# Kernel tuning notes

Hardware: AMD Instinct MI355X
Metric: run time of the kernel (lower is better)

Reference implementation:

```python
import jax, jax.numpy as jnp
import numpy as np

EPS = 1e-5  # torch BatchNorm1d default eps

def _bn(x, g, b, m, v):
    # eval-mode BatchNorm1d with running statistics
    return (x - m) * jax.lax.rsqrt(v + EPS) * g + b

def setup_inputs() -> dict:
    key = jax.random.key(0)
    ks = jax.random.split(key, 6)
    N, E, D = 10000, 320000, 128
    h = jax.random.normal(ks[0], (N, D), dtype=jnp.float32)
    src = jax.random.randint(ks[1], (E,), 0, N)
    dst = jax.random.randint(ks[2], (E,), 0, N)
    # Linear weights (torch layout: [out, in]), kaiming-ish scale
    W0 = jax.random.normal(ks[3], (128, 256), dtype=jnp.float32) * (1.0 / np.sqrt(256))
    b0 = jnp.zeros((128,), jnp.float32)
    W1 = jax.random.normal(ks[4], (128, 128), dtype=jnp.float32) * (1.0 / np.sqrt(128))
    b1 = jnp.zeros((128,), jnp.float32)
    W2 = jax.random.normal(ks[5], (1, 128), dtype=jnp.float32) * (1.0 / np.sqrt(128))
    b2 = jnp.zeros((1,), jnp.float32)
    # BatchNorm affine params + running stats per layer input size
    g0, be0, m0, v0 = jnp.ones((256,)), jnp.zeros((256,)), jnp.zeros((256,)), jnp.ones((256,))
    g1, be1, m1, v1 = jnp.ones((128,)), jnp.zeros((128,)), jnp.zeros((128,)), jnp.ones((128,))
    g2, be2, m2, v2 = jnp.ones((128,)), jnp.zeros((128,)), jnp.zeros((128,)), jnp.ones((128,))
    return dict(h=h, src=src, dst=dst, W0=W0, b0=b0, W1=W1, b1=b1, W2=W2, b2=b2,
                g0=g0, be0=be0, g1=g1, be1=be1, g2=g2, be2=be2,
                m0=m0, v0=v0, m1=m1, v1=v1, m2=m2, v2=v2)

def reference(h, src, dst, W0, b0, W1, b1, W2, b2,
              g0, be0, g1, be1, g2, be2, m0, v0, m1, v1, m2, v2):
    # edge gather + concat: [E, 2*D]
    x = jnp.concatenate([h[src], h[dst]], axis=1)
    # stage 0: BN -> Linear (dropout is identity in eval)
    x = _bn(x, g0, be0, m0, v0) @ W0.T + b0
    # stage 1: ReLU -> BN -> Linear
    x = jax.nn.relu(x)
    x = _bn(x, g1, be1, m1, v1) @ W1.T + b1
    # stage 2: ReLU -> BN -> Linear
    x = jax.nn.relu(x)
    x = _bn(x, g2, be2, m2, v2) @ W2.T + b2
    return x  # [E, 1] edge scores
```

## Files before the change

### kernel.cpp

```cpp
#include <hip/hip_runtime.h>
#include <hip/hip_bf16.h>

#define BN_EPS 1e-5f

typedef short bf16x8 __attribute__((ext_vector_type(8)));
typedef float f32x4  __attribute__((ext_vector_type(4)));

static __device__ __forceinline__ unsigned short f2bf(float f) {
    union { float f; unsigned int u; } v; v.f = f;
    unsigned int u = v.u;
    unsigned int r = (u + 0x7FFFu + ((u >> 16) & 1u)) >> 16;
    return (unsigned short)r;
}

static __device__ __forceinline__ unsigned short f2bf_hw(float f) {
    __hip_bfloat16 b = __float2bfloat16(f);
    union { __hip_bfloat16 b; unsigned short u; } v; v.b = b;
    return v.u;
}

__global__ __launch_bounds__(256) void k_prep(
        const float* __restrict__ h, unsigned short* __restrict__ hb, int n4, int nCvt,
        const float* __restrict__ W0, const float* __restrict__ b0,
        const float* __restrict__ W1, const float* __restrict__ b1,
        const float* __restrict__ W2, const float* __restrict__ b2,
        const float* __restrict__ g0, const float* __restrict__ be0,
        const float* __restrict__ m0, const float* __restrict__ v0,
        const float* __restrict__ g1, const float* __restrict__ be1,
        const float* __restrict__ m1, const float* __restrict__ v1,
        const float* __restrict__ g2, const float* __restrict__ be2,
        const float* __restrict__ m2, const float* __restrict__ v2,
        unsigned short* __restrict__ W0sw, unsigned short* __restrict__ W1sw,
        float* __restrict__ b0f, float* __restrict__ b1f,
        float* __restrict__ w2f, float* __restrict__ b2f) {
    const int b = blockIdx.x;
    const int tid = threadIdx.x;

    if (b < nCvt) {
        int i = b * 256 + tid;
        if (i < n4) {
            float4 f = ((const float4*)h)[i];
            ushort4 o;
            o.x = f2bf(f.x); o.y = f2bf(f.y); o.z = f2bf(f.z); o.w = f2bf(f.w);
            ((ushort4*)hb)[i] = o;
        }
        return;
    }
    int br = b - nCvt;
    if (br < 128) {
        int t = br * 256 + tid;
        int j = t & 7, lane = (t >> 3) & 63, nt = (t >> 9) & 7, kb = t >> 12;
        int k = kb * 32 + (lane >> 4) * 8 + j;
        int n = nt * 16 + (lane & 15);
        float s = g0[k] * rsqrtf(v0[k] + BN_EPS);
        W0sw[t] = f2bf(W0[n * 256 + k] * s);
        return;
    }
    br -= 128;
    if (br < 64) {
        int t = br * 256 + tid;
        int j = t & 7, lane = (t >> 3) & 63, nt = (t >> 9) & 7, kb = t >> 12;
        int k = kb * 32 + (lane >> 4) * 8 + j;
        int n = nt * 16 + (lane & 15);
        float s = g1[k] * rsqrtf(v1[k] + BN_EPS);
        W1sw[t] = f2bf(W1[n * 128 + k] * s);
        return;
    }
    br -= 64;
    {
        if (tid >= 64) return;
        const int i = br, lane = tid;
        float s0 = 0.f;
#pragma unroll
        for (int c = 0; c < 4; c++) {
            int k = c * 64 + lane;
            float sc = g0[k] * rsqrtf(v0[k] + BN_EPS);
            s0 += W0[i * 256 + k] * (be0[k] - m0[k] * sc);
        }
        float s1 = 0.f;
#pragma unroll
        for (int c = 0; c < 2; c++) {
            int k = c * 64 + lane;
            float sc = g1[k] * rsqrtf(v1[k] + BN_EPS);
            s1 += W1[i * 128 + k] * (be1[k] - m1[k] * sc);
        }
        float s2 = 0.f;
        if (i == 0) {
#pragma unroll
            for (int c = 0; c < 2; c++) {
                int k = c * 64 + lane;
                float sc = g2[k] * rsqrtf(v2[k] + BN_EPS);
                s2 += W2[k] * (be2[k] - m2[k] * sc);
            }
        }
#pragma unroll
        for (int off = 1; off < 64; off <<= 1) {
            s0 += __shfl_xor(s0, off);
            s1 += __shfl_xor(s1, off);
            s2 += __shfl_xor(s2, off);
        }
        if (lane == 0) {
            b0f[i] = b0[i] + s0;
            b1f[i] = b1[i] + s1;
            w2f[i] = W2[i] * (g2[i] * rsqrtf(v2[i] + BN_EPS));
            if (i == 0) b2f[0] = b2[0] + s2;
        }
    }
}

__global__ __launch_bounds__(256, 3) void k_main(
        const int* __restrict__ src, const int* __restrict__ dst,
        const unsigned short* __restrict__ hb,
        const unsigned short* __restrict__ W0sw, const unsigned short* __restrict__ W1sw,
        const float* __restrict__ b0f, const float* __restrict__ b1f,
        const float* __restrict__ w2f, const float* __restrict__ b2fp,
        float* __restrict__ out, int E, int nGroups) {
    __shared__ __align__(16) unsigned short Abuf[4 * 2 * 4 * 64 * 8];
    __shared__ __align__(16) unsigned short x1S[4][4][64][8];
    __shared__ float pS[4][64];

    const int tid  = threadIdx.x;
    const int wave = tid >> 6;
    const int lane = tid & 63;
    const int quad = lane >> 4;
    const int m    = lane & 15;

    bf16x8 B0[8][2], B1[4][2];
#pragma unroll
    for (int kb = 0; kb < 8; kb++)
#pragma unroll
        for (int hh = 0; hh < 2; hh++)
            B0[kb][hh] = *(const bf16x8*)(W0sw + ((kb * 8 + (wave * 2 + hh)) * 64 + lane) * 8);
#pragma unroll
    for (int kb = 0; kb < 4; kb++)
#pragma unroll
        for (int hh = 0; hh < 2; hh++)
            B1[kb][hh] = *(const bf16x8*)(W1sw + ((kb * 8 + (wave * 2 + hh)) * 64 + lane) * 8);

    float b0v[2], b1v[2], w2v[2];
#pragma unroll
    for (int hh = 0; hh < 2; hh++) {
        int n = (wave * 2 + hh) * 16 + m;
        b0v[hh] = b0f[n];
        b1v[hh] = b1f[n];
        w2v[hh] = w2f[n];
    }
    const float b2s = *b2fp;
    const int stride = gridDim.x;

    int gi = blockIdx.x;
    int rSn, rDn;
    {
        int e = gi * 64 + wave * 16 + m;
        if (e >= E) e = E - 1;
        rSn = src[e];
        rDn = dst[e];
#pragma unroll
        for (int half = 0; half < 2; half++) {
            int row = half ? rDn : rSn;
#pragma unroll
            for (int kb4 = 0; kb4 < 4; kb4++) {
                const unsigned short* gp = hb + (size_t)row * 128 + kb4 * 32 + quad * 8;
                unsigned short* lp = Abuf + ((wave * 2 + half) * 4 + kb4) * 512 + lane * 8;
                __builtin_amdgcn_global_load_lds(
                    (const __attribute__((address_space(1))) void*)gp,
                    (__attribute__((address_space(3))) void*)lp, 16, 0, 0);
            }
        }
    }

    int prevE = -1;
    for (; gi < nGroups; gi += stride) {
        __syncthreads();

        if (prevE >= 0 && wave == 0) {
            int e = prevE + lane;
            if (e < E)
                out[e] = pS[0][lane] + pS[1][lane] + pS[2][lane] + pS[3][lane] + b2s;
        }

        int nextGi = gi + stride;
        {
            int en = (nextGi < nGroups ? nextGi : gi) * 64 + wave * 16 + m;
            if (en >= E) en = E - 1;
            rSn = src[en];
            rDn = dst[en];
        }

        f32x4 acc0[4][2];
#pragma unroll
        for (int g = 0; g < 4; g++)
#pragma unroll
            for (int hh = 0; hh < 2; hh++) acc0[g][hh] = (f32x4){0.f, 0.f, 0.f, 0.f};

#pragma unroll
        for (int kb = 0; kb < 8; kb++) {
            bf16x8 a[4];
#pragma unroll
            for (int g = 0; g < 4; g++)
                a[g] = *(const bf16x8*)(Abuf + ((g * 2 + (kb >> 2)) * 4 + (kb & 3)) * 512 + lane * 8);
#pragma unroll
            for (int hh = 0; hh < 2; hh++)
#pragma unroll
                for (int g = 0; g < 4; g++)
                    acc0[g][hh] = __builtin_amdgcn_mfma_f32_16x16x32_bf16(a[g], B0[kb][hh], acc0[g][hh], 0, 0, 0);
        }

#pragma unroll
        for (int g = 0; g < 4; g++) {
#pragma unroll
            for (int hh = 0; hh < 2; hh++) {
                int qp = (hh << 1) | (m >> 3);
                int j  = m & 7;
#pragma unroll
                for (int r = 0; r < 4; r++) {
                    float v = acc0[g][hh][r] + b0v[hh];
                    v = v > 0.f ? v : 0.f;
                    x1S[g][wave][qp * 16 + quad * 4 + r][j] = f2bf_hw(v);
                }
            }
        }
        __syncthreads();

        if (nextGi < nGroups) {
#pragma unroll
            for (int half = 0; half < 2; half++) {
                int row = half ? rDn : rSn;
#pragma unroll
                for (int kb4 = 0; kb4 < 4; kb4++) {
                    const unsigned short* gp = hb + (size_t)row * 128 + kb4 * 32 + quad * 8;
                    unsigned short* lp = Abuf + ((wave * 2 + half) * 4 + kb4) * 512 + lane * 8;
                    __builtin_amdgcn_global_load_lds(
                        (const __attribute__((address_space(1))) void*)gp,
                        (__attribute__((address_space(3))) void*)lp, 16, 0, 0);
                }
            }
        }

        f32x4 acc1[4][2];
#pragma unroll
        for (int g = 0; g < 4; g++)
#pragma unroll
            for (int hh = 0; hh < 2; hh++) acc1[g][hh] = (f32x4){0.f, 0.f, 0.f, 0.f};

#pragma unroll
        for (int kb = 0; kb < 4; kb++) {
            bf16x8 a[4];
#pragma unroll
            for (int g = 0; g < 4; g++)
                a[g] = *(const bf16x8*)&x1S[g][kb][lane][0];
#pragma unroll
            for (int hh = 0; hh < 2; hh++)
#pragma unroll
                for (int g = 0; g < 4; g++)
                    acc1[g][hh] = __builtin_amdgcn_mfma_f32_16x16x32_bf16(a[g], B1[kb][hh], acc1[g][hh], 0, 0, 0);
        }

#pragma unroll
        for (int g = 0; g < 4; g++) {
            float s[4] = {0.f, 0.f, 0.f, 0.f};
#pragma unroll
            for (int hh = 0; hh < 2; hh++)
#pragma unroll
                for (int r = 0; r < 4; r++) {
                    float v = acc1[g][hh][r] + b1v[hh];
                    v = v > 0.f ? v : 0.f;
                    s[r] += v * w2v[hh];
                }
#pragma unroll
            for (int off = 1; off < 16; off <<= 1)
#pragma unroll
                for (int r = 0; r < 4; r++) s[r] += __shfl_xor(s[r], off, 16);
            if (m == 0) {
#pragma unroll
                for (int r = 0; r < 4; r++) pS[wave][g * 16 + quad * 4 + r] = s[r];
            }
        }
        prevE = gi * 64;
    }

    __syncthreads();
    if (prevE >= 0 && wave == 0) {
        int e = prevE + lane;
        if (e < E)
            out[e] = pS[0][lane] + pS[1][lane] + pS[2][lane] + pS[3][lane] + b2s;
    }
}

extern "C" void kernel_launch(void* const* d_in, const int* in_sizes, int n_in,
                              void* d_out, int out_size, void* d_ws, size_t ws_size,
                              hipStream_t stream) {
    const float* h   = (const float*)d_in[0];
    const int*   src = (const int*)d_in[1];
    const int*   dst = (const int*)d_in[2];
    const float* W0  = (const float*)d_in[3];
    const float* b0  = (const float*)d_in[4];
    const float* W1  = (const float*)d_in[5];
    const float* b1  = (const float*)d_in[6];
    const float* W2  = (const float*)d_in[7];
    const float* b2  = (const float*)d_in[8];
    const float* g0  = (const float*)d_in[9];
    const float* be0 = (const float*)d_in[10];
    const float* g1  = (const float*)d_in[11];
    const float* be1 = (const float*)d_in[12];
    const float* g2  = (const float*)d_in[13];
    const float* be2 = (const float*)d_in[14];
    const float* m0  = (const float*)d_in[15];
    const float* v0  = (const float*)d_in[16];
    const float* m1  = (const float*)d_in[17];
    const float* v1  = (const float*)d_in[18];
    const float* m2  = (const float*)d_in[19];
    const float* v2  = (const float*)d_in[20];
    float* out = (float*)d_out;

    const int hsz = in_sizes[0];
    const int E   = in_sizes[1];

    char* ws = (char*)d_ws;
    size_t off = (size_t)hsz * 2;
    off = (off + 255) & ~(size_t)255;
    unsigned short* hb   = (unsigned short*)ws;
    unsigned short* W0sw = (unsigned short*)(ws + off);  off += 65536;
    unsigned short* W1sw = (unsigned short*)(ws + off);  off += 32768;
    float* b0f = (float*)(ws + off);  off += 512;
    float* b1f = (float*)(ws + off);  off += 512;
    float* w2f = (float*)(ws + off);  off += 512;
    float* b2f = (float*)(ws + off);  off += 16;

    int n4   = hsz / 4;
    int nCvt = (n4 + 255) / 256;
    int prepBlocks = nCvt + 128 + 64 + 128;
    k_prep<<<prepBlocks, 256, 0, stream>>>(h, hb, n4, nCvt,
                                           W0, b0, W1, b1, W2, b2,
                                           g0, be0, m0, v0, g1, be1, m1, v1,
                                           g2, be2, m2, v2,
                                           W0sw, W1sw, b0f, b1f, w2f, b2f);

    int nGroups = (E + 63) / 64;
    int nBlocks = nGroups < 768 ? nGroups : 768;
    k_main<<<nBlocks, 256, 0, stream>>>(src, dst, hb, W0sw, W1sw,
                                        b0f, b1f, w2f, b2f, out, E, nGroups);
}
```

Before: 143.6 us.

## Process 96 edges per block iteration to amortize register-resident weights

Each block iteration now handles 96 edges (six 16-row groups) instead of 64. Each wave runs MFMAs over all six groups against its register-held W0/W1 slices, and the gather loads are spread so waves 0-1 fetch two groups and waves 2-3 fetch one. Occupancy drops from 3 to 2 blocks per SIMD and the grid from 768 to 512 blocks. The per-edge partial sums now reuse x1S as scratch, with an extra barrier and an immediate write-out in place of the deferred pS write. This should raise MFMA work per barrier and per weight load, at the cost of latency hiding, uneven gather load across waves, and one more sync per iteration.

```diff
diff --git a/kernel.cpp b/kernel.cpp
--- a/kernel.cpp
+++ b/kernel.cpp
@@ -108,16 +108,15 @@
     }
 }
 
-__global__ __launch_bounds__(256, 3) void k_main(
+__global__ __launch_bounds__(256, 2) void k_main(
         const int* __restrict__ src, const int* __restrict__ dst,
         const unsigned short* __restrict__ hb,
         const unsigned short* __restrict__ W0sw, const unsigned short* __restrict__ W1sw,
         const float* __restrict__ b0f, const float* __restrict__ b1f,
         const float* __restrict__ w2f, const float* __restrict__ b2fp,
         float* __restrict__ out, int E, int nGroups) {
-    __shared__ __align__(16) unsigned short Abuf[4 * 2 * 4 * 64 * 8];
-    __shared__ __align__(16) unsigned short x1S[4][4][64][8];
-    __shared__ float pS[4][64];
+    __shared__ __align__(16) unsigned short Abuf[6 * 2 * 4 * 64 * 8];
+    __shared__ __align__(16) unsigned short x1S[6][4][64][8];
 
     const int tid  = threadIdx.x;
     const int wave = tid >> 6;
@@ -148,66 +147,79 @@
     const float b2s = *b2fp;
     const int stride = gridDim.x;
 
+    const int nMyG = (wave < 2) ? 2 : 1;
+    int myG0 = wave, myG1 = 4 + wave;
+
     int gi = blockIdx.x;
-    int rSn, rDn;
+    int rS0, rD0, rS1, rD1;
     {
-        int e = gi * 64 + wave * 16 + m;
-        if (e >= E) e = E - 1;
-        rSn = src[e];
-        rDn = dst[e];
-#pragma unroll
-        for (int half = 0; half < 2; half++) {
-            int row = half ? rDn : rSn;
-#pragma unroll
-            for (int kb4 = 0; kb4 < 4; kb4++) {
-                const unsigned short* gp = hb + (size_t)row * 128 + kb4 * 32 + quad * 8;
-                unsigned short* lp = Abuf + ((wave * 2 + half) * 4 + kb4) * 512 + lane * 8;
-                __builtin_amdgcn_global_load_lds(
-                    (const __attribute__((address_space(1))) void*)gp,
-                    (__attribute__((address_space(3))) void*)lp, 16, 0, 0);
-            }
-        }
-    }
-
-    int prevE = -1;
+        int e0 = gi * 96 + myG0 * 16 + m;
+        if (e0 >= E) e0 = E - 1;
+        rS0 = src[e0]; rD0 = dst[e0];
+        if (nMyG == 2) {
+            int e1 = gi * 96 + myG1 * 16 + m;
+            if (e1 >= E) e1 = E - 1;
+            rS1 = src[e1]; rD1 = dst[e1];
+        }
+#pragma unroll
+        for (int idx = 0; idx < 2; idx++) {
+            if (idx >= nMyG) break;
+            int g  = idx ? myG1 : myG0;
+            int rs = idx ? rS1 : rS0;
+            int rd = idx ? rD1 : rD0;
+#pragma unroll
+            for (int half = 0; half < 2; half++) {
+                int row = half ? rd : rs;
+#pragma unroll
+                for (int kb4 = 0; kb4 < 4; kb4++) {
+                    const unsigned short* gp = hb + (size_t)row * 128 + kb4 * 32 + quad * 8;
+                    unsigned short* lp = Abuf + ((g * 2 + half) * 4 + kb4) * 512 + lane * 8;
+                    __builtin_amdgcn_global_load_lds(
+                        (const __attribute__((address_space(1))) void*)gp,
+                        (__attribute__((address_space(3))) void*)lp, 16, 0, 0);
+                }
+            }
+        }
+    }
+
     for (; gi < nGroups; gi += stride) {
+        const int eBase = gi * 96;
         __syncthreads();
-
-        if (prevE >= 0 && wave == 0) {
-            int e = prevE + lane;
-            if (e < E)
-                out[e] = pS[0][lane] + pS[1][lane] + pS[2][lane] + pS[3][lane] + b2s;
-        }
 
         int nextGi = gi + stride;
         {
-            int en = (nextGi < nGroups ? nextGi : gi) * 64 + wave * 16 + m;
-            if (en >= E) en = E - 1;
-            rSn = src[en];
-            rDn = dst[en];
-        }
-
-        f32x4 acc0[4][2];
-#pragma unroll
-        for (int g = 0; g < 4; g++)
+            int eb = (nextGi < nGroups ? nextGi : gi) * 96;
+            int e0 = eb + myG0 * 16 + m;
+            if (e0 >= E) e0 = E - 1;
+            rS0 = src[e0]; rD0 = dst[e0];
+            if (nMyG == 2) {
+                int e1 = eb + myG1 * 16 + m;
+                if (e1 >= E) e1 = E - 1;
+                rS1 = src[e1]; rD1 = dst[e1];
+            }
+        }
+
+        f32x4 acc0[6][2];
+#pragma unroll
+        for (int g = 0; g < 6; g++)
 #pragma unroll
             for (int hh = 0; hh < 2; hh++) acc0[g][hh] = (f32x4){0.f, 0.f, 0.f, 0.f};
 
 #pragma unroll
         for (int kb = 0; kb < 8; kb++) {
-            bf16x8 a[4];
-#pragma unroll
-            for (int g = 0; g < 4; g++)
+            bf16x8 a[6];
+#pragma unroll
+            for (int g = 0; g < 6; g++)
                 a[g] = *(const bf16x8*)(Abuf + ((g * 2 + (kb >> 2)) * 4 + (kb & 3)) * 512 + lane * 8);
 #pragma unroll
             for (int hh = 0; hh < 2; hh++)
 #pragma unroll
-                for (int g = 0; g < 4; g++)
+                for (int g = 0; g < 6; g++)
                     acc0[g][hh] = __builtin_amdgcn_mfma_f32_16x16x32_bf16(a[g], B0[kb][hh], acc0[g][hh], 0, 0, 0);
         }
 
 #pragma unroll
-        for (int g = 0; g < 4; g++) {
+        for (int g = 0; g < 6; g++) {
 #pragma unroll
             for (int hh = 0; hh < 2; hh++) {
                 int qp = (hh << 1) | (m >> 3);
@@ -224,40 +236,47 @@
 
         if (nextGi < nGroups) {
 #pragma unroll
-            for (int half = 0; half < 2; half++) {
-                int row = half ? rDn : rSn;
-#pragma unroll
-                for (int kb4 = 0; kb4 < 4; kb4++) {
-                    const unsigned short* gp = hb + (size_t)row * 128 + kb4 * 32 + quad * 8;
-                    unsigned short* lp = Abuf + ((wave * 2 + half) * 4 + kb4) * 512 + lane * 8;
-                    __builtin_amdgcn_global_load_lds(
-                        (const __attribute__((address_space(1))) void*)gp,
-                        (__attribute__((address_space(3))) void*)lp, 16, 0, 0);
+            for (int idx = 0; idx < 2; idx++) {
+                if (idx >= nMyG) break;
+                int g  = idx ? myG1 : myG0;
+                int rs = idx ? rS1 : rS0;
+                int rd = idx ? rD1 : rD0;
+#pragma unroll
+                for (int half = 0; half < 2; half++) {
+                    int row = half ? rd : rs;
+#pragma unroll
+                    for (int kb4 = 0; kb4 < 4; kb4++) {
+                        const unsigned short* gp = hb + (size_t)row * 128 + kb4 * 32 + quad * 8;
+                        unsigned short* lp = Abuf + ((g * 2 + half) * 4 + kb4) * 512 + lane * 8;
+                        __builtin_amdgcn_global_load_lds(
+                            (const __attribute__((address_space(1))) void*)gp,
+                            (__attribute__((address_space(3))) void*)lp, 16, 0, 0);
+                    }
                 }
             }
         }
 
-        f32x4 acc1[4][2];
-#pragma unroll
-        for (int g = 0; g < 4; g++)
+        f32x4 acc1[6][2];
+#pragma unroll
+        for (int g = 0; g < 6; g++)
 #pragma unroll
             for (int hh = 0; hh < 2; hh++) acc1[g][hh] = (f32x4){0.f, 0.f, 0.f, 0.f};
 
 #pragma unroll
         for (int kb = 0; kb < 4; kb++) {
-            bf16x8 a[4];
-#pragma unroll
-            for (int g = 0; g < 4; g++)
+            bf16x8 a[6];
+#pragma unroll
+            for (int g = 0; g < 6; g++)
                 a[g] = *(const bf16x8*)&x1S[g][kb][lane][0];
 #pragma unroll
             for (int hh = 0; hh < 2; hh++)
 #pragma unroll
-                for (int g = 0; g < 4; g++)
+                for (int g = 0; g < 6; g++)
                     acc1[g][hh] = __builtin_amdgcn_mfma_f32_16x16x32_bf16(a[g], B1[kb][hh], acc1[g][hh], 0, 0, 0);
         }
 
 #pragma unroll
-        for (int g = 0; g < 4; g++) {
+        for (int g = 0; g < 6; g++) {
             float s[4] = {0.f, 0.f, 0.f, 0.f};
 #pragma unroll
             for (int hh = 0; hh < 2; hh++)
@@ -272,18 +291,23 @@
 #pragma unroll
                 for (int r = 0; r < 4; r++) s[r] += __shfl_xor(s[r], off, 16);
             if (m == 0) {
-#pragma unroll
-                for (int r = 0; r < 4; r++) pS[wave][g * 16 + quad * 4 + r] = s[r];
-            }
-        }
-        prevE = gi * 64;
-    }
-
-    __syncthreads();
-    if (prevE >= 0 && wave == 0) {
-        int e = prevE + lane;
-        if (e < E)
-            out[e] = pS[0][lane] + pS[1][lane] + pS[2][lane] + pS[3][lane] + b2s;
+                float* pS = (float*)&x1S[0][0][0][0];
+                pS[(wave * 6 + g) * 16 + quad * 4 + 0] = s[0];
+                pS[(wave * 6 + g) * 16 + quad * 4 + 1] = s[1];
+                pS[(wave * 6 + g) * 16 + quad * 4 + 2] = s[2];
+                pS[(wave * 6 + g) * 16 + quad * 4 + 3] = s[3];
+            }
+        }
+        __syncthreads();
+        {
+            int eo = wave * 64 + lane;
+            if (wave < 2 && eo < 96) {
+                const float* pS = (const float*)&x1S[0][0][0][0];
+                int e = eBase + eo;
+                if (e < E)
+                    out[e] = pS[0 * 96 + eo] + pS[1 * 96 + eo] + pS[2 * 96 + eo] + pS[3 * 96 + eo] + b2s;
+            }
+        }
     }
 }
 
@@ -336,8 +360,8 @@
                                            g2, be2, m2, v2,
                                            W0sw, W1sw, b0f, b1f, w2f, b2f);
 
-    int nGroups = (E + 63) / 64;
-    int nBlocks = nGroups < 768 ? nGroups : 768;
+    int nGroups = (E + 95) / 96;
+    int nBlocks = nGroups < 512 ? nGroups : 512;
     k_main<<<nBlocks, 256, 0, stream>>>(src, dst, hb, W0sw, W1sw,
                                         b0f, b1f, w2f, b2f, out, E, nGroups);
 }
```

New measurement: 149.1 us. 3.8% more time.

## Software-pipeline layer-0 and layer-1 across iterations with double-buffered LDS

Applied to the files above, without the earlier changes.

Restructures the main loop into a two-stage software pipeline. Each iteration runs layer-0 MFMAs for the current edge group and layer-1 for the previous group, using double-buffered A tiles, hidden activations and partial sums. That removes one __syncthreads per iteration, and the gather DMA for the next group is issued before compute rather than mid-iteration. Group size drops to 48 edges (3 MFMA row tiles) to fit the doubled LDS, with occupancy lowered to 2 blocks/SM and grid to 512. The trade-off is fewer edges per MFMA batch, lower occupancy, and prologue/epilogue complexity.

```diff
diff --git a/kernel.cpp b/kernel.cpp
--- a/kernel.cpp
+++ b/kernel.cpp
@@ -2,6 +2,8 @@
 #include <hip/hip_bf16.h>
 
 #define BN_EPS 1e-5f
+#define MG 3
+#define GEDGES 48
 
 typedef short bf16x8 __attribute__((ext_vector_type(8)));
 typedef float f32x4  __attribute__((ext_vector_type(4)));
@@ -108,16 +110,35 @@
     }
 }
 
-__global__ __launch_bounds__(256, 3) void k_main(
+static __device__ __forceinline__ void dma_issue(
+        unsigned short* AbufBase, const unsigned short* __restrict__ hb,
+        int wave, int lane, int quad, int rowS, int rowD) {
+    const int gIdx = (wave < 2) ? wave : 2;
+    const int h0 = (wave == 3) ? 1 : 0;
+    const int h1 = (wave < 2) ? 1 : h0;
+    for (int half = h0; half <= h1; half++) {
+        int row = half ? rowD : rowS;
+#pragma unroll
+        for (int kb4 = 0; kb4 < 4; kb4++) {
+            const unsigned short* gp = hb + (size_t)row * 128 + kb4 * 32 + quad * 8;
+            unsigned short* lp = AbufBase + ((gIdx * 2 + half) * 4 + kb4) * 512 + lane * 8;
+            __builtin_amdgcn_global_load_lds(
+                (const __attribute__((address_space(1))) void*)gp,
+                (__attribute__((address_space(3))) void*)lp, 16, 0, 0);
+        }
+    }
+}
+
+__global__ __launch_bounds__(256, 2) void k_main(
         const int* __restrict__ src, const int* __restrict__ dst,
         const unsigned short* __restrict__ hb,
         const unsigned short* __restrict__ W0sw, const unsigned short* __restrict__ W1sw,
         const float* __restrict__ b0f, const float* __restrict__ b1f,
         const float* __restrict__ w2f, const float* __restrict__ b2fp,
         float* __restrict__ out, int E, int nGroups) {
-    __shared__ __align__(16) unsigned short Abuf[4 * 2 * 4 * 64 * 8];
-    __shared__ __align__(16) unsigned short x1S[4][4][64][8];
-    __shared__ float pS[4][64];
+    __shared__ __align__(16) unsigned short Abuf[2][MG * 2 * 4 * 64 * 8];
+    __shared__ __align__(16) unsigned short x1S[2][MG][4][64][8];
+    __shared__ float pS[2][4][GEDGES];
 
     const int tid  = threadIdx.x;
     const int wave = tid >> 6;
@@ -147,67 +168,64 @@
     }
     const float b2s = *b2fp;
     const int stride = gridDim.x;
+    const int gIdx = (wave < 2) ? wave : 2;
 
     int gi = blockIdx.x;
-    int rSn, rDn;
+    int p = 0;
+    int eM1 = -1, eM2 = -1;
+    int rNS, rND;
+
     {
-        int e = gi * 64 + wave * 16 + m;
-        if (e >= E) e = E - 1;
-        rSn = src[e];
-        rDn = dst[e];
-#pragma unroll
-        for (int half = 0; half < 2; half++) {
-            int row = half ? rDn : rSn;
-#pragma unroll
-            for (int kb4 = 0; kb4 < 4; kb4++) {
-                const unsigned short* gp = hb + (size_t)row * 128 + kb4 * 32 + quad * 8;
-                unsigned short* lp = Abuf + ((wave * 2 + half) * 4 + kb4) * 512 + lane * 8;
-                __builtin_amdgcn_global_load_lds(
-                    (const __attribute__((address_space(1))) void*)gp,
-                    (__attribute__((address_space(3))) void*)lp, 16, 0, 0);
-            }
-        }
-    }
-
-    int prevE = -1;
-    for (; gi < nGroups; gi += stride) {
+        int eb = gi * GEDGES;
+        int e = eb + gIdx * 16 + m; if (e >= E) e = E - 1;
+        int rs = src[e], rd = dst[e];
+        dma_issue(&Abuf[0][0], hb, wave, lane, quad, rs, rd);
+        int gN = gi + stride;
+        int ebN = (gN < nGroups ? gN : gi) * GEDGES;
+        int eN = ebN + gIdx * 16 + m; if (eN >= E) eN = E - 1;
+        rNS = src[eN]; rND = dst[eN];
+    }
+
+    for (; gi < nGroups; gi += stride, p ^= 1) {
         __syncthreads();
 
-        if (prevE >= 0 && wave == 0) {
-            int e = prevE + lane;
+        if (eM2 >= 0 && wave == 0 && lane < GEDGES) {
+            int e = eM2 + lane;
             if (e < E)
-                out[e] = pS[0][lane] + pS[1][lane] + pS[2][lane] + pS[3][lane] + b2s;
-        }
-
-        int nextGi = gi + stride;
+                out[e] = pS[p ^ 1][0][lane] + pS[p ^ 1][1][lane] +
+                         pS[p ^ 1][2][lane] + pS[p ^ 1][3][lane] + b2s;
+        }
+
+        if (gi + stride < nGroups)
+            dma_issue(&Abuf[p ^ 1][0], hb, wave, lane, quad, rNS, rND);
+
         {
-            int en = (nextGi < nGroups ? nextGi : gi) * 64 + wave * 16 + m;
-            if (en >= E) en = E - 1;
-            rSn = src[en];
-            rDn = dst[en];
-        }
-
-        f32x4 acc0[4][2];
-#pragma unroll
-        for (int g = 0; g < 4; g++)
+            int g2i = gi + 2 * stride;
+            int eb2 = (g2i < nGroups ? g2i : gi) * GEDGES;
+            int e2 = eb2 + gIdx * 16 + m; if (e2 >= E) e2 = E - 1;
+            rNS = src[e2]; rND = dst[e2];
+        }
+
+        f32x4 acc0[MG][2];
+#pragma unroll
+        for (int g = 0; g < MG; g++)
 #pragma unroll
             for (int hh = 0; hh < 2; hh++) acc0[g][hh] = (f32x4){0.f, 0.f, 0.f, 0.f};
 
 #pragma unroll
         for (int kb = 0; kb < 8; kb++) {
-            bf16x8 a[4];
-#pragma unroll
-            for (int g = 0; g < 4; g++)
-                a[g] = *(const bf16x8*)(Abuf + ((g * 2 + (kb >> 2)) * 4 + (kb & 3)) * 512 + lane * 8);
+            bf16x8 a[MG];
+#pragma unroll
+            for (int g = 0; g < MG; g++)
+                a[g] = *(const bf16x8*)(&Abuf[p][((g * 2 + (kb >> 2)) * 4 + (kb & 3)) * 512 + lane * 8]);
 #pragma unroll
             for (int hh = 0; hh < 2; hh++)
 #pragma unroll
-                for (int g = 0; g < 4; g++)
+                for (int g = 0; g < MG; g++)
                     acc0[g][hh] = __builtin_amdgcn_mfma_f32_16x16x32_bf16(a[g], B0[kb][hh], acc0[g][hh], 0, 0, 0);
         }
-
-#pragma unroll
-        for (int g = 0; g < 4; g++) {
+#pragma unroll
+        for (int g = 0; g < MG; g++) {
 #pragma unroll
             for (int hh = 0; hh < 2; hh++) {
                 int qp = (hh << 1) | (m >> 3);
@@ -216,48 +234,84 @@
                 for (int r = 0; r < 4; r++) {
                     float v = acc0[g][hh][r] + b0v[hh];
                     v = v > 0.f ? v : 0.f;
-                    x1S[g][wave][qp * 16 + quad * 4 + r][j] = f2bf_hw(v);
+                    x1S[p][g][wave][qp * 16 + quad * 4 + r][j] = f2bf_hw(v);
                 }
             }
         }
-        __syncthreads();
-
-        if (nextGi < nGroups) {
-#pragma unroll
-            for (int half = 0; half < 2; half++) {
-                int row = half ? rDn : rSn;
-#pragma unroll
-                for (int kb4 = 0; kb4 < 4; kb4++) {
-                    const unsigned short* gp = hb + (size_t)row * 128 + kb4 * 32 + quad * 8;
-                    unsigned short* lp = Abuf + ((wave * 2 + half) * 4 + kb4) * 512 + lane * 8;
-                    __builtin_amdgcn_global_load_lds(
-                        (const __attribute__((address_space(1))) void*)gp,
-                        (__attribute__((address_space(3))) void*)lp, 16, 0, 0);
+
+        if (eM1 >= 0) {
+            f32x4 acc1[MG][2];
+#pragma unroll
+            for (int g = 0; g < MG; g++)
+#pragma unroll
+                for (int hh = 0; hh < 2; hh++) acc1[g][hh] = (f32x4){0.f, 0.f, 0.f, 0.f};
+
+#pragma unroll
+            for (int kb = 0; kb < 4; kb++) {
+                bf16x8 a[MG];
+#pragma unroll
+                for (int g = 0; g < MG; g++)
+                    a[g] = *(const bf16x8*)&x1S[p ^ 1][g][kb][lane][0];
+#pragma unroll
+                for (int hh = 0; hh < 2; hh++)
+#pragma unroll
+                    for (int g = 0; g < MG; g++)
+                        acc1[g][hh] = __builtin_amdgcn_mfma_f32_16x16x32_bf16(a[g], B1[kb][hh], acc1[g][hh], 0, 0, 0);
+            }
+#pragma unroll
+            for (int g = 0; g < MG; g++) {
+                float s[4] = {0.f, 0.f, 0.f, 0.f};
+#pragma unroll
+                for (int hh = 0; hh < 2; hh++)
+#pragma unroll
+                    for (int r = 0; r < 4; r++) {
+                        float v = acc1[g][hh][r] + b1v[hh];
+                        v = v > 0.f ? v : 0.f;
+                        s[r] += v * w2v[hh];
+                    }
+#pragma unroll
+                for (int off = 1; off < 16; off <<= 1)
+#pragma unroll
+                    for (int r = 0; r < 4; r++) s[r] += __shfl_xor(s[r], off, 16);
+                if (m == 0) {
+#pragma unroll
+                    for (int r = 0; r < 4; r++)
+                        pS[p][wave][g * 16 + quad * 4 + r] = s[r];
                 }
             }
         }
 
-        f32x4 acc1[4][2];
-#pragma unroll
-        for (int g = 0; g < 4; g++)
+        eM2 = eM1;
+        eM1 = gi * GEDGES;
+    }
+
+    __syncthreads();
+    if (eM2 >= 0 && wave == 0 && lane < GEDGES) {
+        int e = eM2 + lane;
+        if (e < E)
+            out[e] = pS[p ^ 1][0][lane] + pS[p ^ 1][1][lane] +
+                     pS[p ^ 1][2][lane] + pS[p ^ 1][3][lane] + b2s;
+    }
+    if (eM1 >= 0) {
+        f32x4 acc1[MG][2];
+#pragma unroll
+        for (int g = 0; g < MG; g++)
 #pragma unroll
             for (int hh = 0; hh < 2; hh++) acc1[g][hh] = (f32x4){0.f, 0.f, 0.f, 0.f};
-
 #pragma unroll
         for (int kb = 0; kb < 4; kb++) {
-            bf16x8 a[4];
-#pragma unroll
-            for (int g = 0; g < 4; g++)
-                a[g] = *(const bf16x8*)&x1S[g][kb][lane][0];
+            bf16x8 a[MG];
+#pragma unroll
+            for (int g = 0; g < MG; g++)
+                a[g] = *(const bf16x8*)&x1S[p ^ 1][g][kb][lane][0];
 #pragma unroll
             for (int hh = 0; hh < 2; hh++)
 #pragma unroll
-                for (int g = 0; g < 4; g++)
+                for (int g = 0; g < MG; g++)
                     acc1[g][hh] = __builtin_amdgcn_mfma_f32_16x16x32_bf16(a[g], B1[kb][hh], acc1[g][hh], 0, 0, 0);
         }
-
-#pragma unroll
-        for (int g = 0; g < 4; g++) {
+#pragma unroll
+        for (int g = 0; g < MG; g++) {
             float s[4] = {0.f, 0.f, 0.f, 0.f};
 #pragma unroll
             for (int hh = 0; hh < 2; hh++)
@@ -273,17 +327,17 @@
                 for (int r = 0; r < 4; r++) s[r] += __shfl_xor(s[r], off, 16);
             if (m == 0) {
 #pragma unroll
-                for (int r = 0; r < 4; r++) pS[wave][g * 16 + quad * 4 + r] = s[r];
-            }
-        }
-        prevE = gi * 64;
-    }
-
+                for (int r = 0; r < 4; r++)
+                    pS[p][wave][g * 16 + quad * 4 + r] = s[r];
+            }
+        }
+    }
     __syncthreads();
-    if (prevE >= 0 && wave == 0) {
-        int e = prevE + lane;
+    if (eM1 >= 0 && wave == 0 && lane < GEDGES) {
+        int e = eM1 + lane;
         if (e < E)
-            out[e] = pS[0][lane] + pS[1][lane] + pS[2][lane] + pS[3][lane] + b2s;
+            out[e] = pS[p][0][lane] + pS[p][1][lane] +
+                     pS[p][2][lane] + pS[p][3][lane] + b2s;
     }
 }
 
@@ -336,8 +390,8 @@
                                            g2, be2, m2, v2,
                                            W0sw, W1sw, b0f, b1f, w2f, b2f);
 
-    int nGroups = (E + 63) / 64;
-    int nBlocks = nGroups < 768 ? nGroups : 768;
+    int nGroups = (E + GEDGES - 1) / GEDGES;
+    int nBlocks = nGroups < 512 ? nGroups : 512;
     k_main<<<nBlocks, 256, 0, stream>>>(src, dst, hb, W0sw, W1sw,
                                         b0f, b1f, w2f, b2f, out, E, nGroups);
 }
```

After: 146.2 us. Within noise of the previous version (+1.8%).
